# Kernel tuning notes

Measured on AMD Instinct MI355X. Metric: run time of the kernel, lower is better.

The kernel has to match this reference:

```python
import jax, jax.numpy as jnp
import numpy as np

B, S, D, H = 8, 1024, 1024, 16
HD = D // H  # head_dim = 64
SCALE = HD ** -0.5


def setup_inputs() -> dict:
    key = jax.random.key(0)
    ks = jax.random.split(key, 10)
    std = D ** -0.5
    return {
        "hidden_states": jax.random.normal(ks[0], (B, S, D), jnp.float32),
        "attn_mask": jnp.zeros((B, 1, S, S), jnp.float32),
        "prev_attn_weights": jax.random.normal(ks[1], (B, H, S, S), jnp.float32),
        "Wq": jax.random.normal(ks[2], (D, D), jnp.float32) * std,
        "bq": jnp.zeros((D,), jnp.float32),
        "Wk": jax.random.normal(ks[3], (D, D), jnp.float32) * std,
        "bk": jnp.zeros((D,), jnp.float32),
        "Wv": jax.random.normal(ks[4], (D, D), jnp.float32) * std,
        "bv": jnp.zeros((D,), jnp.float32),
    }


def _split_heads(x):
    # (B, S, D) -> (B, H, S, HD)
    return x.reshape(B, S, H, HD).transpose(0, 2, 1, 3)


def reference(hidden_states, attn_mask, prev_attn_weights, Wq, bq, Wk, bk, Wv, bv):
    q = _split_heads(hidden_states @ Wq + bq)
    k = _split_heads(hidden_states @ Wk + bk)
    v = _split_heads(hidden_states @ Wv + bv)
    # scaled dot-product scores + additive mask + realformer residual scores
    scores = jnp.einsum("bhqd,bhkd->bhqk", q, k) * SCALE
    scores = scores + attn_mask + prev_attn_weights
    probs = jax.nn.softmax(scores, axis=-1)  # dropout p=0 (eval)
    ctx = jnp.einsum("bhqk,bhkd->bhqd", probs, v)
    # (B, H, S, HD) -> (B, S, D)
    out = ctx.transpose(0, 2, 1, 3).reshape(B, S, D)
    return out
```

## Files before the change

### kernel.cpp

```cpp
#include <hip/hip_runtime.h>

#define B_  8
#define S_  1024
#define D_  1024
#define H_  16
#define HD_ 64
#define M_  8192
#define LOG2E 1.44269504088896f
#define QSCALE_ (0.125f * 1.44269504088896f)
#define MSHIFT_ 20.0f

typedef __attribute__((ext_vector_type(8))) short bf16x8;
typedef __attribute__((ext_vector_type(4))) float f32x4;

__device__ __forceinline__ unsigned short f2b(float x) {
  union { float f; unsigned u; } un; un.f = x;
  unsigned r = un.u + 0x7FFFu + ((un.u >> 16) & 1u);
  return (unsigned short)(r >> 16);
}

__global__ __launch_bounds__(256) void k_convert_x(const float* __restrict__ x,
                                                   unsigned short* __restrict__ o) {
  int i = (blockIdx.x * 256 + threadIdx.x) * 4;
  const int n = M_ * D_;
  const int stride = gridDim.x * 256 * 4;
  for (; i < n; i += stride) {
    const float4 v = *(const float4*)(x + i);
    ushort4 r;
    r.x = f2b(v.x); r.y = f2b(v.y); r.z = f2b(v.z); r.w = f2b(v.w);
    *(ushort4*)(o + i) = r;
  }
}

__global__ __launch_bounds__(256) void k_transpose_w(const float* __restrict__ Wq,
    const float* __restrict__ Wk, const float* __restrict__ Wv,
    unsigned short* __restrict__ Wt) {
  __shared__ float t[64][65];
  const float* W = (blockIdx.z == 0) ? Wq : ((blockIdx.z == 1) ? Wk : Wv);
  unsigned short* dst = Wt + (size_t)blockIdx.z * (D_ * D_);
  const int k0 = blockIdx.x * 64, n0 = blockIdx.y * 64;
  const int tid = threadIdx.x;
#pragma unroll
  for (int i = 0; i < 16; ++i) {
    const int lin = i * 256 + tid;
    const int r = lin >> 6, c = lin & 63;
    t[r][c] = W[(size_t)(k0 + r) * D_ + n0 + c];
  }
  __syncthreads();
#pragma unroll
  for (int i = 0; i < 16; ++i) {
    const int lin = i * 256 + tid;
    const int r = lin >> 6, c = lin & 63;
    dst[(size_t)(n0 + r) * D_ + k0 + c] = f2b(t[c][r]);
  }
}

template <int MODE>
__global__ __launch_bounds__(256) void k_proj(const unsigned short* __restrict__ X,
    const unsigned short* __restrict__ Wt,
    const float* __restrict__ bq, const float* __restrict__ bk, const float* __restrict__ bv,
    unsigned short* __restrict__ Qw, unsigned short* __restrict__ Kw,
    unsigned short* __restrict__ Vt) {
  __shared__ unsigned short xs[128 * 32];
  __shared__ unsigned short wsh[128 * 32];
  const int tid = threadIdx.x;
  const int lane = tid & 63, wv = tid >> 6;
  const int g = lane >> 4, li = lane & 15;
  const int m0 = blockIdx.x * 128;
  const int n0 = blockIdx.y * 128;
  const int wr = wv >> 1, wc = wv & 1;
  const int wtrow0 = (MODE == 0) ? n0 : (2048 + n0);

  f32x4 acc[4][4];
#pragma unroll
  for (int i = 0; i < 4; ++i)
#pragma unroll
    for (int j = 0; j < 4; ++j) acc[i][j] = (f32x4){0.f, 0.f, 0.f, 0.f};

  const int srow = wv * 32 + (lane >> 2);
  const int skel = (lane & 3) * 8;

  for (int k0 = 0; k0 < D_; k0 += 32) {
#pragma unroll
    for (int i = 0; i < 2; ++i) {
      const unsigned short* gx = X + (size_t)(m0 + srow + i * 16) * D_ + k0 + skel;
      const unsigned short* gw = Wt + (size_t)(wtrow0 + srow + i * 16) * D_ + k0 + skel;
      __builtin_amdgcn_global_load_lds(
          (const __attribute__((address_space(1))) void*)gx,
          (__attribute__((address_space(3))) void*)&xs[(wv * 32 + i * 16) * 32], 16, 0, 0);
      __builtin_amdgcn_global_load_lds(
          (const __attribute__((address_space(1))) void*)gw,
          (__attribute__((address_space(3))) void*)&wsh[(wv * 32 + i * 16) * 32], 16, 0, 0);
    }
    __syncthreads();
    bf16x8 af[4], bfr[4];
#pragma unroll
    for (int i = 0; i < 4; ++i) {
      const int ar = wr * 64 + i * 16 + li;
      const int br = wc * 64 + i * 16 + li;
      if (MODE == 0) {
        af[i]  = *(const bf16x8*)&xs[ar * 32 + g * 8];
        bfr[i] = *(const bf16x8*)&wsh[br * 32 + g * 8];
      } else {
        af[i]  = *(const bf16x8*)&wsh[ar * 32 + g * 8];
        bfr[i] = *(const bf16x8*)&xs[br * 32 + g * 8];
      }
    }
#pragma unroll
    for (int i = 0; i < 4; ++i)
#pragma unroll
      for (int j = 0; j < 4; ++j)
        acc[i][j] = __builtin_amdgcn_mfma_f32_16x16x32_bf16(af[i], bfr[j], acc[i][j], 0, 0, 0);
    __syncthreads();
  }

  if (MODE == 0) {
#pragma unroll
    for (int j = 0; j < 4; ++j) {
      const int n = n0 + wc * 64 + j * 16 + li;
      const float bias = (n < D_) ? bq[n] : bk[n - D_];
#pragma unroll
      for (int i = 0; i < 4; ++i) {
#pragma unroll
        for (int r = 0; r < 4; ++r) {
          const int m = m0 + wr * 64 + i * 16 + g * 4 + r;
          const float v = acc[i][j][r] + bias;
          const int bb = m >> 10, ss = m & 1023;
          if (n < D_) {
            Qw[((size_t)(bb * H_ + (n >> 6)) * S_ + ss) * HD_ + (n & 63)] = f2b(v * QSCALE_);
          } else {
            const int nk = n - D_;
            Kw[((size_t)(bb * H_ + (nk >> 6)) * S_ + ss) * HD_ + (nk & 63)] = f2b(v);
          }
        }
      }
    }
  } else {
#pragma unroll
    for (int i = 0; i < 4; ++i) {
#pragma unroll
      for (int r = 0; r < 4; ++r) {
        const int nv = n0 + wr * 64 + i * 16 + g * 4 + r;
        const float bias = bv[nv];
#pragma unroll
        for (int j = 0; j < 4; ++j) {
          const int m = m0 + wc * 64 + j * 16 + li;
          const int bb = m >> 10, ss = m & 1023;
          const float v = acc[i][j][r] + bias;
          Vt[((size_t)(bb * H_ + (nv >> 6)) * HD_ + (nv & 63)) * S_ + ss] = f2b(v);
        }
      }
    }
  }
}

__global__ __launch_bounds__(256, 2) void k_attn(const unsigned short* __restrict__ Qw,
    const unsigned short* __restrict__ Kw, const unsigned short* __restrict__ Vt,
    const float* __restrict__ prev, const float* __restrict__ mask,
    float* __restrict__ out) {
  __shared__ unsigned short k_s[2][4096];
  __shared__ unsigned short v_s[2][4096];
  __shared__ float pm_s[2][4][4][64][4];
  __shared__ unsigned short p_lds[4][16][72];
  const int tid = threadIdx.x;
  const int lane = tid & 63, wv = tid >> 6;
  const int g = lane >> 4, li = lane & 15;

  const int phys = blockIdx.x + 16 * blockIdx.y;
  const int xcd = phys & 7, idx = phys >> 3;
  const int qt = idx & 15;
  const int bh = xcd + 8 * (idx >> 4);
  const int b = bh >> 4, h = bh & 15;
  const int q0 = qt * 64 + wv * 16;

  const float* pdma = prev + (size_t)bh * S_ * S_ + (size_t)(q0 + li) * S_ + g * 4;
  const float* mb   = mask + (size_t)b * S_ * S_ + (size_t)(q0 + li) * S_ + g * 4;
  const unsigned short* kbase = Kw + (size_t)bh * S_ * HD_;
  const unsigned short* vbase = Vt + (size_t)bh * HD_ * S_;

  bf16x8 qf[2];
  {
    const unsigned short* qp = Qw + ((size_t)bh * S_ + q0 + li) * HD_ + g * 8;
    qf[0] = *(const bf16x8*)qp;
    qf[1] = *(const bf16x8*)(qp + 32);
  }

  const int dr0 = (0 * 256 + tid) >> 3, dc0 = (0 * 256 + tid) & 7;
  const int dr1 = (1 * 256 + tid) >> 3, dc1 = (1 * 256 + tid) & 7;
  const int sc0 = ((dc0 ^ (dr0 & 7)) << 3);
  const int sc1 = ((dc1 ^ (dr1 & 7)) << 3);

#define STAGE(TN, BI)                                                                      \
  {                                                                                        \
    const int sn = (TN) * 64;                                                              \
    __builtin_amdgcn_global_load_lds(                                                      \
        (const __attribute__((address_space(1))) void*)(kbase + (size_t)(sn + dr0) * HD_ + sc0), \
        (__attribute__((address_space(3))) void*)(&k_s[BI][0] + wv * 512), 16, 0, 0);      \
    __builtin_amdgcn_global_load_lds(                                                      \
        (const __attribute__((address_space(1))) void*)(kbase + (size_t)(sn + dr1) * HD_ + sc1), \
        (__attribute__((address_space(3))) void*)(&k_s[BI][0] + 2048 + wv * 512), 16, 0, 0); \
    __builtin_amdgcn_global_load_lds(                                                      \
        (const __attribute__((address_space(1))) void*)(vbase + (size_t)dr0 * S_ + sn + sc0), \
        (__attribute__((address_space(3))) void*)(&v_s[BI][0] + wv * 512), 16, 0, 0);      \
    __builtin_amdgcn_global_load_lds(                                                      \
        (const __attribute__((address_space(1))) void*)(vbase + (size_t)dr1 * S_ + sn + sc1), \
        (__attribute__((address_space(3))) void*)(&v_s[BI][0] + 2048 + wv * 512), 16, 0, 0); \
    _Pragma("unroll")                                                                      \
    for (int cb = 0; cb < 4; ++cb)                                                         \
      __builtin_amdgcn_global_load_lds(                                                    \
          (const __attribute__((address_space(1))) void*)(pdma + sn + cb * 16),            \
          (__attribute__((address_space(3))) void*)&pm_s[BI][wv][cb][0][0], 16, 0, 0);     \
  }

  float lrun = 0.f;
  f32x4 ctx[4];
#pragma unroll
  for (int d = 0; d < 4; ++d) ctx[d] = (f32x4){0.f, 0.f, 0.f, 0.f};

  STAGE(0, 0);
  __syncthreads();

  int cur = 0;
  for (int t = 0; t < 16; ++t) {
    f32x4 mA[4];
#pragma unroll
    for (int cb = 0; cb < 4; ++cb) mA[cb] = *(const f32x4*)(mb + t * 64 + cb * 16);

    if (t < 15) STAGE(t + 1, cur ^ 1);

    const unsigned short* kb = &k_s[cur][0];
    const unsigned short* vb = &v_s[cur][0];
    f32x4 sa[4];
#pragma unroll
    for (int cb = 0; cb < 4; ++cb) {
      const int r = cb * 16 + li;
      const bf16x8 k0 = *(const bf16x8*)(kb + r * 64 + ((g ^ (li & 7)) << 3));
      const bf16x8 k1 = *(const bf16x8*)(kb + r * 64 + (((g + 4) ^ (li & 7)) << 3));
      f32x4 z = (f32x4){0.f, 0.f, 0.f, 0.f};
      z      = __builtin_amdgcn_mfma_f32_16x16x32_bf16(k0, qf[0], z, 0, 0, 0);
      sa[cb] = __builtin_amdgcn_mfma_f32_16x16x32_bf16(k1, qf[1], z, 0, 0, 0);
    }

#pragma unroll
    for (int cb = 0; cb < 4; ++cb) {
      const f32x4 pv = *(const f32x4*)&pm_s[cur][wv][cb][lane][0];
      f32x4 pmc;
      pmc.x = fmaf(pv.x + mA[cb].x, LOG2E, -MSHIFT_);
      pmc.y = fmaf(pv.y + mA[cb].y, LOG2E, -MSHIFT_);
      pmc.z = fmaf(pv.z + mA[cb].z, LOG2E, -MSHIFT_);
      pmc.w = fmaf(pv.w + mA[cb].w, LOG2E, -MSHIFT_);
      const float e0 = exp2f(sa[cb][0] + pmc.x);
      const float e1 = exp2f(sa[cb][1] + pmc.y);
      const float e2 = exp2f(sa[cb][2] + pmc.z);
      const float e3 = exp2f(sa[cb][3] + pmc.w);
      lrun += (e0 + e1) + (e2 + e3);
      ushort4 pw;
      pw.x = f2b(e0); pw.y = f2b(e1); pw.z = f2b(e2); pw.w = f2b(e3);
      *(ushort4*)&p_lds[wv][li][cb * 16 + g * 4] = pw;
    }

    bf16x8 pf0 = *(const bf16x8*)&p_lds[wv][li][g * 8];
    bf16x8 pf1 = *(const bf16x8*)&p_lds[wv][li][32 + g * 8];
#pragma unroll
    for (int d = 0; d < 4; ++d) {
      const int r = d * 16 + li;
      const bf16x8 v0 = *(const bf16x8*)(vb + r * 64 + ((g ^ (li & 7)) << 3));
      const bf16x8 v1 = *(const bf16x8*)(vb + r * 64 + (((g + 4) ^ (li & 7)) << 3));
      ctx[d] = __builtin_amdgcn_mfma_f32_16x16x32_bf16(pf0, v0, ctx[d], 0, 0, 0);
      ctx[d] = __builtin_amdgcn_mfma_f32_16x16x32_bf16(pf1, v1, ctx[d], 0, 0, 0);
    }

    __syncthreads();
    cur ^= 1;
  }
#undef STAGE

  lrun += __shfl_xor(lrun, 16);
  lrun += __shfl_xor(lrun, 32);
#pragma unroll
  for (int j = 0; j < 4; ++j) {
    const float rs = __shfl(lrun, g * 4 + j);
    const float inv = 1.0f / rs;
    const int q = q0 + g * 4 + j;
    float* op = out + ((size_t)b * S_ + q) * D_ + h * HD_ + li;
#pragma unroll
    for (int d = 0; d < 4; ++d)
      op[d * 16] = ctx[d][j] * inv;
  }
}

extern "C" void kernel_launch(void* const* d_in, const int* in_sizes, int n_in,
                              void* d_out, int out_size, void* d_ws, size_t ws_size,
                              hipStream_t stream) {
  const float* hs   = (const float*)d_in[0];
  const float* mask = (const float*)d_in[1];
  const float* prev = (const float*)d_in[2];
  const float* Wq   = (const float*)d_in[3];
  const float* bq   = (const float*)d_in[4];
  const float* Wk   = (const float*)d_in[5];
  const float* bk   = (const float*)d_in[6];
  const float* Wv   = (const float*)d_in[7];
  const float* bv   = (const float*)d_in[8];
  float* out = (float*)d_out;

  char* ws = (char*)d_ws;
  unsigned short* Xbf = (unsigned short*)ws;
  unsigned short* Wt  = (unsigned short*)(ws + (16ull << 20));
  unsigned short* Qw  = (unsigned short*)(ws + (22ull << 20));
  unsigned short* Kw  = (unsigned short*)(ws + (38ull << 20));
  unsigned short* Vt  = (unsigned short*)(ws + (54ull << 20));

  k_convert_x<<<2048, 256, 0, stream>>>(hs, Xbf);
  k_transpose_w<<<dim3(16, 16, 3), 256, 0, stream>>>(Wq, Wk, Wv, Wt);
  k_proj<0><<<dim3(64, 16), 256, 0, stream>>>(Xbf, Wt, bq, bk, bv, Qw, Kw, Vt);
  k_proj<1><<<dim3(64, 8),  256, 0, stream>>>(Xbf, Wt, bq, bk, bv, Qw, Kw, Vt);
  k_attn<<<dim3(16, 128), 256, 0, stream>>>(Qw, Kw, Vt, prev, mask, out);
}
```

Baseline: 317.9 us.

## Keep next-tile loads in flight with partial vmcnt waits and raw barriers

Restructures the attention K/V/prev-score loop into an unrolled two-phase ping-pong. Each phase issues the next tile's async global-to-LDS loads and mask loads, then waits only until the older batch completes (vmcnt(12)) before the barrier, rather than a full __syncthreads drain. The mask values are also prefetched one tile ahead into alternating registers. The aim is to overlap global loads with MFMA/exp work. It risks correctness if the vmcnt count doesn't match the issued load count, and it redundantly re-stages tile 15 on the last iteration.

```diff
diff --git a/kernel.cpp b/kernel.cpp
--- a/kernel.cpp
+++ b/kernel.cpp
@@ -217,62 +217,70 @@
 #pragma unroll
   for (int d = 0; d < 4; ++d) ctx[d] = (f32x4){0.f, 0.f, 0.f, 0.f};
 
+  f32x4 mA[4], mB[4];
+
   STAGE(0, 0);
-  __syncthreads();
-
-  int cur = 0;
-  for (int t = 0; t < 16; ++t) {
-    f32x4 mA[4];
-#pragma unroll
-    for (int cb = 0; cb < 4; ++cb) mA[cb] = *(const f32x4*)(mb + t * 64 + cb * 16);
-
-    if (t < 15) STAGE(t + 1, cur ^ 1);
-
-    const unsigned short* kb = &k_s[cur][0];
-    const unsigned short* vb = &v_s[cur][0];
-    f32x4 sa[4];
-#pragma unroll
-    for (int cb = 0; cb < 4; ++cb) {
-      const int r = cb * 16 + li;
-      const bf16x8 k0 = *(const bf16x8*)(kb + r * 64 + ((g ^ (li & 7)) << 3));
-      const bf16x8 k1 = *(const bf16x8*)(kb + r * 64 + (((g + 4) ^ (li & 7)) << 3));
-      f32x4 z = (f32x4){0.f, 0.f, 0.f, 0.f};
-      z      = __builtin_amdgcn_mfma_f32_16x16x32_bf16(k0, qf[0], z, 0, 0, 0);
-      sa[cb] = __builtin_amdgcn_mfma_f32_16x16x32_bf16(k1, qf[1], z, 0, 0, 0);
-    }
-
-#pragma unroll
-    for (int cb = 0; cb < 4; ++cb) {
-      const f32x4 pv = *(const f32x4*)&pm_s[cur][wv][cb][lane][0];
-      f32x4 pmc;
-      pmc.x = fmaf(pv.x + mA[cb].x, LOG2E, -MSHIFT_);
-      pmc.y = fmaf(pv.y + mA[cb].y, LOG2E, -MSHIFT_);
-      pmc.z = fmaf(pv.z + mA[cb].z, LOG2E, -MSHIFT_);
-      pmc.w = fmaf(pv.w + mA[cb].w, LOG2E, -MSHIFT_);
-      const float e0 = exp2f(sa[cb][0] + pmc.x);
-      const float e1 = exp2f(sa[cb][1] + pmc.y);
-      const float e2 = exp2f(sa[cb][2] + pmc.z);
-      const float e3 = exp2f(sa[cb][3] + pmc.w);
-      lrun += (e0 + e1) + (e2 + e3);
-      ushort4 pw;
-      pw.x = f2b(e0); pw.y = f2b(e1); pw.z = f2b(e2); pw.w = f2b(e3);
-      *(ushort4*)&p_lds[wv][li][cb * 16 + g * 4] = pw;
-    }
-
-    bf16x8 pf0 = *(const bf16x8*)&p_lds[wv][li][g * 8];
-    bf16x8 pf1 = *(const bf16x8*)&p_lds[wv][li][32 + g * 8];
-#pragma unroll
-    for (int d = 0; d < 4; ++d) {
-      const int r = d * 16 + li;
-      const bf16x8 v0 = *(const bf16x8*)(vb + r * 64 + ((g ^ (li & 7)) << 3));
-      const bf16x8 v1 = *(const bf16x8*)(vb + r * 64 + (((g + 4) ^ (li & 7)) << 3));
-      ctx[d] = __builtin_amdgcn_mfma_f32_16x16x32_bf16(pf0, v0, ctx[d], 0, 0, 0);
-      ctx[d] = __builtin_amdgcn_mfma_f32_16x16x32_bf16(pf1, v1, ctx[d], 0, 0, 0);
-    }
-
-    __syncthreads();
-    cur ^= 1;
-  }
+#pragma unroll
+  for (int cb = 0; cb < 4; ++cb) mA[cb] = *(const f32x4*)(mb + cb * 16);
+
+#define PHASE(T, PB, NB, MCUR, MNXT)                                                  \
+  {                                                                                   \
+    const int tn = ((T) < 15) ? (T) + 1 : 15;                                         \
+    STAGE(tn, NB);                                                                    \
+    _Pragma("unroll")                                                                 \
+    for (int cb = 0; cb < 4; ++cb)                                                    \
+      MNXT[cb] = *(const f32x4*)(mb + tn * 64 + cb * 16);                             \
+    asm volatile("s_waitcnt vmcnt(12)" ::: "memory");                                 \
+    __builtin_amdgcn_s_barrier();                                                     \
+    {                                                                                 \
+      const unsigned short* kb = &k_s[PB][0];                                         \
+      const unsigned short* vb = &v_s[PB][0];                                         \
+      f32x4 sa[4];                                                                    \
+      _Pragma("unroll")                                                               \
+      for (int cb = 0; cb < 4; ++cb) {                                                \
+        const int r = cb * 16 + li;                                                   \
+        const bf16x8 k0 = *(const bf16x8*)(kb + r * 64 + ((g ^ (li & 7)) << 3));      \
+        const bf16x8 k1 = *(const bf16x8*)(kb + r * 64 + (((g + 4) ^ (li & 7)) << 3)); \
+        f32x4 z = (f32x4){0.f, 0.f, 0.f, 0.f};                                        \
+        z      = __builtin_amdgcn_mfma_f32_16x16x32_bf16(k0, qf[0], z, 0, 0, 0);      \
+        sa[cb] = __builtin_amdgcn_mfma_f32_16x16x32_bf16(k1, qf[1], z, 0, 0, 0);      \
+      }                                                                               \
+      _Pragma("unroll")                                                               \
+      for (int cb = 0; cb < 4; ++cb) {                                                \
+        const f32x4 pv = *(const f32x4*)&pm_s[PB][wv][cb][lane][0];                   \
+        f32x4 pmc;                                                                    \
+        pmc.x = fmaf(pv.x + MCUR[cb].x, LOG2E, -MSHIFT_);                             \
+        pmc.y = fmaf(pv.y + MCUR[cb].y, LOG2E, -MSHIFT_);                             \
+        pmc.z = fmaf(pv.z + MCUR[cb].z, LOG2E, -MSHIFT_);                             \
+        pmc.w = fmaf(pv.w + MCUR[cb].w, LOG2E, -MSHIFT_);                             \
+        const float e0 = exp2f(sa[cb][0] + pmc.x);                                    \
+        const float e1 = exp2f(sa[cb][1] + pmc.y);                                    \
+        const float e2 = exp2f(sa[cb][2] + pmc.z);                                    \
+        const float e3 = exp2f(sa[cb][3] + pmc.w);                                    \
+        lrun += (e0 + e1) + (e2 + e3);                                                \
+        ushort4 pw;                                                                   \
+        pw.x = f2b(e0); pw.y = f2b(e1); pw.z = f2b(e2); pw.w = f2b(e3);               \
+        *(ushort4*)&p_lds[wv][li][cb * 16 + g * 4] = pw;                              \
+      }                                                                               \
+      bf16x8 pf0 = *(const bf16x8*)&p_lds[wv][li][g * 8];                             \
+      bf16x8 pf1 = *(const bf16x8*)&p_lds[wv][li][32 + g * 8];                        \
+      _Pragma("unroll")                                                               \
+      for (int d = 0; d < 4; ++d) {                                                   \
+        const int r = d * 16 + li;                                                    \
+        const bf16x8 v0 = *(const bf16x8*)(vb + r * 64 + ((g ^ (li & 7)) << 3));      \
+        const bf16x8 v1 = *(const bf16x8*)(vb + r * 64 + (((g + 4) ^ (li & 7)) << 3)); \
+        ctx[d] = __builtin_amdgcn_mfma_f32_16x16x32_bf16(pf0, v0, ctx[d], 0, 0, 0);   \
+        ctx[d] = __builtin_amdgcn_mfma_f32_16x16x32_bf16(pf1, v1, ctx[d], 0, 0, 0);   \
+      }                                                                               \
+    }                                                                                 \
+    __builtin_amdgcn_s_barrier();                                                     \
+  }
+
+  for (int t = 0; t < 16; t += 2) {
+    PHASE(t,     0, 1, mA, mB);
+    PHASE(t + 1, 1, 0, mB, mA);
+  }
+#undef PHASE
 #undef STAGE
 
   lrun += __shfl_xor(lrun, 16);
```

New measurement: 285.0 us. -10.3%, faster.
